# Kernel optimization log

Hardware: AMD Instinct MI355X
Metric: run time of the kernel (lower is better)

The kernel has to match this reference:

```python
import jax, jax.numpy as jnp
import numpy as np

B = 256          # batch_size (number of graphs)
N = 512          # padded nodes per graph
IN_FEATS = 74
DIM = 128
E = 1_048_576    # total edges in batched graph
N_NODES = B * N


def setup_inputs() -> dict:
    key = jax.random.key(0)
    ks = jax.random.split(key, 10)
    x = jax.random.normal(ks[0], (N_NODES, IN_FEATS), dtype=jnp.float32)
    src = jax.random.randint(ks[1], (E,), 0, N_NODES, dtype=jnp.int32)
    dst = jax.random.randint(ks[2], (E,), 0, N_NODES, dtype=jnp.int32)
    # init_transform: Linear(in_feats, dim_embedding, bias=False); padding=True
    # zeroes weight[-1] (last OUTPUT row) -> last column in [in, out] layout.
    W_init = jax.random.normal(ks[3], (IN_FEATS, DIM), dtype=jnp.float32) * 0.1
    W_init = W_init.at[:, -1].set(0.0)
    W1 = jax.random.normal(ks[4], (DIM, DIM), dtype=jnp.float32) * 0.1
    W2 = jax.random.normal(ks[5], (DIM, DIM), dtype=jnp.float32) * 0.1
    W3 = jax.random.normal(ks[6], (DIM, DIM), dtype=jnp.float32) * 0.1
    b1 = jnp.zeros((DIM,), dtype=jnp.float32)
    b2 = jnp.zeros((DIM,), dtype=jnp.float32)
    b3 = jnp.zeros((DIM,), dtype=jnp.float32)
    return {"x": x, "src": src, "dst": dst, "W_init": W_init,
            "W1": W1, "b1": b1, "W2": W2, "b2": b2, "W3": W3, "b3": b3}


def _gcn_forward(x, src, dst, W_init, Ws, bs):
    n = x.shape[0]
    h = x @ W_init                                    # [n, DIM] initial embedding
    ones = jnp.ones(src.shape[0], dtype=x.dtype)
    deg_out = jax.ops.segment_sum(ones, src, num_segments=n)
    deg_in = jax.ops.segment_sum(ones, dst, num_segments=n)
    nrm_src = jax.lax.rsqrt(jnp.clip(deg_out, 1.0))   # D_out^{-1/2}
    nrm_dst = jax.lax.rsqrt(jnp.clip(deg_in, 1.0))    # D_in^{-1/2}
    for W, b in zip(Ws, bs):
        m = (h * nrm_src[:, None])[src]               # gather normalized messages [E, DIM]
        agg = jax.ops.segment_sum(m, dst, num_segments=n)  # scatter-add to dst nodes
        h = jax.nn.relu((agg * nrm_dst[:, None]) @ W + b)
    return h.reshape(B, N, -1)                        # [B, N, output_feats]


def reference(x, src, dst, W_init, W1, b1, W2, b2, W3, b3):
    return _gcn_forward(x, src, dst, W_init, (W1, W2, W3), (b1, b2, b3))
```

## Files before the change

### kernel.cpp

```cpp
#include <hip/hip_runtime.h>

#define NN 131072
#define NE 1048576
#define OFF_DEG_OUT 0x000000
#define OFF_CURSOR  0x080000
#define OFF_WT      0x100000
#define OFF_WTI     0x118000
#define OFF_BUCKET  0x200000
#define OFF_HN      0x2200000
#define OFF_SCA     0x3200000
#define OFF_SCB     0x3280000

typedef __attribute__((ext_vector_type(8))) short bf16x8;
typedef __attribute__((ext_vector_type(4))) float f32x4;

static __device__ __forceinline__ float blo(unsigned u){ return __uint_as_float(u << 16); }
static __device__ __forceinline__ float bhi(unsigned u){ return __uint_as_float(u & 0xffff0000u); }
static __device__ __forceinline__ unsigned f2b(float f){
    unsigned u = __float_as_uint(f);
    return (u + 0x7fffu + ((u >> 16) & 1u)) >> 16;
}
static __device__ __forceinline__ unsigned pack2(float a, float b){
    return f2b(a) | (f2b(b) << 16);
}
static __device__ __forceinline__ unsigned packq(int q0, int q1, int q2, int q3){
    return (q0 & 255) | ((q1 & 255) << 8) | ((q2 & 255) << 16) | ((q3 & 255) << 24);
}

__global__ __launch_bounds__(256) void k_wprep(const float* __restrict__ W1,
                                               const float* __restrict__ W2,
                                               const float* __restrict__ W3,
                                               const float* __restrict__ Wi,
                                               unsigned short* __restrict__ Wt,
                                               unsigned short* __restrict__ Wti,
                                               uint4* __restrict__ zdst) {
    int idx = blockIdx.x * 256 + threadIdx.x;
    zdst[idx] = (uint4){0u, 0u, 0u, 0u};
    if (idx < 49152) {
        int L = idx >> 14, rem = idx & 16383;
        int k = rem >> 7, n = rem & 127;
        const float* W = L == 0 ? W1 : (L == 1 ? W2 : W3);
        Wt[L * 16384 + n * 128 + k] = (unsigned short)f2b(W[k * 128 + n]);
    } else if (idx < 61440) {
        int rem = idx - 49152;
        int n = rem / 96, k = rem - n * 96;
        float v = (k < 74) ? Wi[k * 128 + n] : 0.f;
        Wti[n * 96 + k] = (unsigned short)f2b(v);
    }
}

__global__ __launch_bounds__(256) void k_pre(const int* __restrict__ src,
                                             const int* __restrict__ dst,
                                             int* __restrict__ deg_out,
                                             int* __restrict__ cursor,
                                             int* __restrict__ bucket,
                                             const float* __restrict__ X,
                                             const unsigned short* __restrict__ Wti,
                                             unsigned char* __restrict__ hn,
                                             float* __restrict__ scInv) {
    __shared__ unsigned int xs[64 * 68];
    int tid = threadIdx.x;

    if (!(blockIdx.x & 1)) {
        int base = ((blockIdx.x >> 1) * 256 + tid) * 2;
        int2 s2 = *(const int2*)&src[base];
        int2 d2 = *(const int2*)&dst[base];
        int p0 = atomicAdd(&cursor[d2.x], 1);
        int p1 = atomicAdd(&cursor[d2.y], 1);
        atomicAdd(&deg_out[s2.x], 1);
        atomicAdd(&deg_out[s2.y], 1);
        if (p0 < 64) bucket[(size_t)d2.x * 64 + p0] = s2.x;
        if (p1 < 64) bucket[(size_t)d2.y * 64 + p1] = s2.y;
        return;
    }

    int m0 = (blockIdx.x >> 1) * 64;

    for (int idx = tid; idx < 2368; idx += 256) {
        int m = idx / 37, t = idx - m * 37;
        float2 v = *(const float2*)&X[(size_t)(m0 + m) * 74 + t * 2];
        xs[m * 68 + t] = pack2(v.x, v.y);
    }
    for (int idx = tid; idx < 64 * 11; idx += 256) {
        int m = idx / 11, c = 37 + idx % 11;
        xs[m * 68 + c] = 0u;
    }
    __syncthreads();

    int wave = tid >> 6, lane = tid & 63, quad = lane >> 4, l16 = lane & 15;
    f32x4 acc[8];
    #pragma unroll
    for (int t = 0; t < 8; ++t) acc[t] = (f32x4){0.f, 0.f, 0.f, 0.f};
    int arow = (wave * 16 + l16) * 68 + quad * 4;
    #pragma unroll
    for (int ks = 0; ks < 3; ++ks) {
        bf16x8 af = *(const bf16x8*)&xs[arow + ks * 16];
        #pragma unroll
        for (int t = 0; t < 8; ++t) {
            bf16x8 bf = *(const bf16x8*)(Wti + (t * 16 + l16) * 96 + ks * 32 + quad * 8);
            acc[t] = __builtin_amdgcn_mfma_f32_16x16x32_bf16(af, bf, acc[t], 0, 0, 0);
        }
    }
    __syncthreads();
    unsigned short* atb = (unsigned short*)xs;
    int mb = wave * 16 + quad * 4;
    #pragma unroll
    for (int t = 0; t < 8; ++t)
        #pragma unroll
        for (int r = 0; r < 4; ++r)
            atb[(mb + r) * 136 + t * 16 + l16] = (unsigned short)f2b(acc[t][r]);
    __syncthreads();
    {
        int r = tid >> 2, cg = tid & 3;
        const unsigned int* sp = &xs[r * 68 + cg * 16];
        float v[32]; float am = 0.f;
        #pragma unroll
        for (int j = 0; j < 16; ++j) {
            unsigned u = sp[j];
            float e = blo(u), o = bhi(u);
            v[2 * j] = e; v[2 * j + 1] = o;
            am = fmaxf(am, fmaxf(fabsf(e), fabsf(o)));
        }
        am = fmaxf(am, __shfl_xor(am, 1));
        am = fmaxf(am, __shfl_xor(am, 2));
        float scl = am > 1e-30f ? 127.f / am : 0.f;
        if (cg == 0) scInv[m0 + r] = am * (1.f / 127.f);
        unsigned w[8];
        #pragma unroll
        for (int j = 0; j < 8; ++j)
            w[j] = packq((int)rintf(v[4 * j] * scl),     (int)rintf(v[4 * j + 1] * scl),
                         (int)rintf(v[4 * j + 2] * scl), (int)rintf(v[4 * j + 3] * scl));
        uint4* op = (uint4*)(hn + (size_t)(m0 + r) * 128 + cg * 32);
        op[0] = (uint4){w[0], w[1], w[2], w[3]};
        op[1] = (uint4){w[4], w[5], w[6], w[7]};
    }
}

__global__ __launch_bounds__(256) void k_scnorm(float* __restrict__ sc,
                                                const int* __restrict__ deg) {
    int i = blockIdx.x * 256 + threadIdx.x;
    int d = deg[i];
    sc[i] *= rsqrtf((float)(d > 1 ? d : 1));
}

#define DEQS8(vv, ss) do {                                                     \
    unsigned ux = (vv).x, uy = (vv).y;                                         \
    a0 = fmaf((ss), (float)(int)(signed char)(ux),       a0);                  \
    a1 = fmaf((ss), (float)(int)(signed char)(ux >> 8),  a1);                  \
    a2 = fmaf((ss), (float)(int)(signed char)(ux >> 16), a2);                  \
    a3 = fmaf((ss), (float)(int)(signed char)(ux >> 24), a3);                  \
    a4 = fmaf((ss), (float)(int)(signed char)(uy),       a4);                  \
    a5 = fmaf((ss), (float)(int)(signed char)(uy >> 8),  a5);                  \
    a6 = fmaf((ss), (float)(int)(signed char)(uy >> 16), a6);                  \
    a7 = fmaf((ss), (float)(int)(signed char)(uy >> 24), a7);                  \
} while (0)

#define DEQU8(vv, ss) do {                                                     \
    unsigned ux = (vv).x, uy = (vv).y;                                         \
    a0 = fmaf((ss), (float)(ux & 255),         a0);                            \
    a1 = fmaf((ss), (float)((ux >> 8) & 255),  a1);                            \
    a2 = fmaf((ss), (float)((ux >> 16) & 255), a2);                            \
    a3 = fmaf((ss), (float)(ux >> 24),         a3);                            \
    a4 = fmaf((ss), (float)(uy & 255),         a4);                            \
    a5 = fmaf((ss), (float)((uy >> 8) & 255),  a5);                            \
    a6 = fmaf((ss), (float)((uy >> 16) & 255), a6);                            \
    a7 = fmaf((ss), (float)(uy >> 24),         a7);                            \
} while (0)

template<int USRC>
__global__ __launch_bounds__(256) void k_layer(const uint2* __restrict__ hn2,
                                               const float* __restrict__ sc,
                                               const int* __restrict__ bucket,
                                               const int* __restrict__ deg_in,
                                               const int* __restrict__ deg_out,
                                               const unsigned short* __restrict__ Wt,
                                               const float* __restrict__ bias,
                                               void* __restrict__ OutP,
                                               float* __restrict__ scOut, int last) {
    __shared__ unsigned int at[64 * 68];
    int tid = threadIdx.x;
    int m0 = blockIdx.x * 64;

    int g = tid >> 4, l16p = tid & 15;
    #pragma unroll
    for (int pass = 0; pass < 4; ++pass) {
        int nl = pass * 16 + g;
        int n = m0 + nl;
        int cnt = deg_in[n];
        cnt = cnt < 64 ? cnt : 64;
        const int* brow = bucket + (size_t)n * 64;
        float a0 = 0, a1 = 0, a2 = 0, a3 = 0, a4 = 0, a5 = 0, a6 = 0, a7 = 0;
        for (int c = 0; c < cnt; c += 8) {
            int4 sA = *(const int4*)&brow[c];
            int4 sB = *(const int4*)&brow[c + 4];
            int lim = cnt - c;
            int i1 = lim > 1 ? sA.y : 0;
            int i2 = lim > 2 ? sA.z : 0;
            int i3 = lim > 3 ? sA.w : 0;
            int i4 = lim > 4 ? sB.x : 0;
            int i5 = lim > 5 ? sB.y : 0;
            int i6 = lim > 6 ? sB.z : 0;
            int i7 = lim > 7 ? sB.w : 0;
            uint2 v0 = hn2[(size_t)sA.x * 16 + l16p];
            uint2 v1 = hn2[(size_t)i1 * 16 + l16p];
            uint2 v2 = hn2[(size_t)i2 * 16 + l16p];
            uint2 v3 = hn2[(size_t)i3 * 16 + l16p];
            uint2 v4 = hn2[(size_t)i4 * 16 + l16p];
            uint2 v5 = hn2[(size_t)i5 * 16 + l16p];
            uint2 v6 = hn2[(size_t)i6 * 16 + l16p];
            uint2 v7 = hn2[(size_t)i7 * 16 + l16p];
            float s0 = sc[sA.x];
            float s1 = sc[i1]; s1 = lim > 1 ? s1 : 0.f;
            float s2 = sc[i2]; s2 = lim > 2 ? s2 : 0.f;
            float s3 = sc[i3]; s3 = lim > 3 ? s3 : 0.f;
            float s4 = sc[i4]; s4 = lim > 4 ? s4 : 0.f;
            float s5 = sc[i5]; s5 = lim > 5 ? s5 : 0.f;
            float s6 = sc[i6]; s6 = lim > 6 ? s6 : 0.f;
            float s7 = sc[i7]; s7 = lim > 7 ? s7 : 0.f;
            if (USRC) {
                DEQU8(v0, s0); DEQU8(v1, s1); DEQU8(v2, s2); DEQU8(v3, s3);
                DEQU8(v4, s4); DEQU8(v5, s5); DEQU8(v6, s6); DEQU8(v7, s7);
            } else {
                DEQS8(v0, s0); DEQS8(v1, s1); DEQS8(v2, s2); DEQS8(v3, s3);
                DEQS8(v4, s4); DEQS8(v5, s5); DEQS8(v6, s6); DEQS8(v7, s7);
            }
        }
        float nd = rsqrtf((float)(cnt > 1 ? cnt : 1));
        uint4 o;
        o.x = pack2(a0 * nd, a1 * nd); o.y = pack2(a2 * nd, a3 * nd);
        o.z = pack2(a4 * nd, a5 * nd); o.w = pack2(a6 * nd, a7 * nd);
        *(uint4*)&at[nl * 68 + l16p * 4] = o;
    }
    __syncthreads();

    f32x4 acc[8];
    #pragma unroll
    for (int t = 0; t < 8; ++t) acc[t] = (f32x4){0.f, 0.f, 0.f, 0.f};
    int wave = tid >> 6, lane = tid & 63, quad = lane >> 4, l16 = lane & 15;
    int arow = (wave * 16 + l16) * 68 + quad * 4;
    #pragma unroll
    for (int ks = 0; ks < 4; ++ks) {
        bf16x8 af = *(const bf16x8*)&at[arow + ks * 16];
        #pragma unroll
        for (int t = 0; t < 8; ++t) {
            bf16x8 bf = *(const bf16x8*)(Wt + (t * 16 + l16) * 128 + ks * 32 + quad * 8);
            acc[t] = __builtin_amdgcn_mfma_f32_16x16x32_bf16(af, bf, acc[t], 0, 0, 0);
        }
    }

    int mb = wave * 16 + quad * 4;
    if (!last) {
        float nsr[4];
        #pragma unroll
        for (int r = 0; r < 4; ++r) {
            int dq = deg_out[m0 + mb + r];
            nsr[r] = rsqrtf((float)(dq > 1 ? dq : 1));
        }
        __syncthreads();
        unsigned short* atb = (unsigned short*)at;
        #pragma unroll
        for (int t = 0; t < 8; ++t) {
            float bv = bias[t * 16 + l16];
            #pragma unroll
            for (int r = 0; r < 4; ++r) {
                float v = acc[t][r] + bv;
                v = (v > 0.f ? v : 0.f) * nsr[r];
                atb[(mb + r) * 136 + t * 16 + l16] = (unsigned short)f2b(v);
            }
        }
        __syncthreads();
        int r = tid >> 2, cg = tid & 3;
        const unsigned int* sp = &at[r * 68 + cg * 16];
        float v[32]; float am = 0.f;
        #pragma unroll
        for (int j = 0; j < 16; ++j) {
            unsigned u = sp[j];
            float e = blo(u), o = bhi(u);
            v[2 * j] = e; v[2 * j + 1] = o;
            am = fmaxf(am, fmaxf(e, o));
        }
        am = fmaxf(am, __shfl_xor(am, 1));
        am = fmaxf(am, __shfl_xor(am, 2));
        float scl = am > 1e-30f ? 254.f / am : 0.f;
        if (cg == 0) scOut[m0 + r] = am * (1.f / 254.f);
        unsigned w[8];
        #pragma unroll
        for (int j = 0; j < 8; ++j)
            w[j] = packq((int)rintf(v[4 * j] * scl),     (int)rintf(v[4 * j + 1] * scl),
                         (int)rintf(v[4 * j + 2] * scl), (int)rintf(v[4 * j + 3] * scl));
        unsigned char* Out = (unsigned char*)OutP;
        uint4* op = (uint4*)(Out + (size_t)(m0 + r) * 128 + cg * 32);
        op[0] = (uint4){w[0], w[1], w[2], w[3]};
        op[1] = (uint4){w[4], w[5], w[6], w[7]};
    } else {
        float* Out = (float*)OutP;
        #pragma unroll
        for (int t = 0; t < 8; ++t) {
            float bv = bias[t * 16 + l16];
            #pragma unroll
            for (int r = 0; r < 4; ++r) {
                float v = acc[t][r] + bv;
                v = v > 0.f ? v : 0.f;
                Out[(size_t)(m0 + mb + r) * 128 + t * 16 + l16] = v;
            }
        }
    }
}

extern "C" void kernel_launch(void* const* d_in, const int* in_sizes, int n_in,
                              void* d_out, int out_size, void* d_ws, size_t ws_size,
                              hipStream_t stream) {
    const float* x  = (const float*)d_in[0];
    const int* src  = (const int*)d_in[1];
    const int* dst  = (const int*)d_in[2];
    const float* Wi = (const float*)d_in[3];
    const float* W1 = (const float*)d_in[4];
    const float* b1 = (const float*)d_in[5];
    const float* W2 = (const float*)d_in[6];
    const float* b2 = (const float*)d_in[7];
    const float* W3 = (const float*)d_in[8];
    const float* b3 = (const float*)d_in[9];

    char* ws = (char*)d_ws;
    int* deg_out   = (int*)(ws + OFF_DEG_OUT);
    int* cursor    = (int*)(ws + OFF_CURSOR);
    unsigned short* Wt  = (unsigned short*)(ws + OFF_WT);
    unsigned short* Wti = (unsigned short*)(ws + OFF_WTI);
    int* bucket    = (int*)(ws + OFF_BUCKET);
    unsigned char* hnA = (unsigned char*)(ws + OFF_HN);
    float* scA     = (float*)(ws + OFF_SCA);
    float* scB     = (float*)(ws + OFF_SCB);
    unsigned char* hnB = (unsigned char*)d_out;

    k_wprep<<<256, 256, 0, stream>>>(W1, W2, W3, Wi, Wt, Wti, (uint4*)ws);
    k_pre<<<4096, 256, 0, stream>>>(src, dst, deg_out, cursor, bucket, x, Wti, hnA, scA);
    k_scnorm<<<NN / 256, 256, 0, stream>>>(scA, deg_out);

    k_layer<0><<<NN / 64, 256, 0, stream>>>((const uint2*)hnA, scA, bucket, cursor, deg_out,
                                            Wt,         b1, (void*)hnB, scB, 0);
    k_layer<1><<<NN / 64, 256, 0, stream>>>((const uint2*)hnB, scB, bucket, cursor, deg_out,
                                            Wt + 16384, b2, (void*)hnA, scA, 0);
    k_layer<1><<<NN / 64, 256, 0, stream>>>((const uint2*)hnA, scA, bucket, cursor, deg_out,
                                            Wt + 32768, b3, d_out, nullptr, 1);
}
```

Baseline: 392.1 us.

## Requantize features to a global scale to drop per-source scale gathers

```diff
diff --git a/kernel.cpp b/kernel.cpp
--- a/kernel.cpp
+++ b/kernel.cpp
@@ -8,8 +8,9 @@
 #define OFF_WTI     0x118000
 #define OFF_BUCKET  0x200000
 #define OFF_HN      0x2200000
-#define OFF_SCA     0x3200000
-#define OFF_SCB     0x3280000
+#define OFF_SCA     0x3210000
+#define OFF_SCB     0x3290000
+#define OFF_GMAX    0x3310000
 
 typedef __attribute__((ext_vector_type(8))) short bf16x8;
 typedef __attribute__((ext_vector_type(4))) float f32x4;
@@ -33,9 +34,19 @@
                                                const float* __restrict__ Wi,
                                                unsigned short* __restrict__ Wt,
                                                unsigned short* __restrict__ Wti,
-                                               uint4* __restrict__ zdst) {
+                                               uint4* __restrict__ zdst,
+                                               unsigned char* __restrict__ hnA,
+                                               unsigned char* __restrict__ hnB,
+                                               unsigned int* __restrict__ gmax) {
     int idx = blockIdx.x * 256 + threadIdx.x;
     zdst[idx] = (uint4){0u, 0u, 0u, 0u};
+    if (blockIdx.x == 255) {
+        int t = threadIdx.x;
+        uint4 z = (uint4){0u, 0u, 0u, 0u};
+        if (t < 8)        ((uint4*)(hnA + (size_t)NN * 128))[t] = z;
+        else if (t < 16)  ((uint4*)(hnB + (size_t)NN * 128))[t - 8] = z;
+        else if (t == 16) { gmax[0] = 0u; gmax[1] = 0u; gmax[2] = 0u; }
+    }
     if (idx < 49152) {
         int L = idx >> 14, rem = idx & 16383;
         int k = rem >> 7, n = rem & 127;
@@ -136,50 +147,98 @@
     }
 }
 
-__global__ __launch_bounds__(256) void k_scnorm(float* __restrict__ sc,
-                                                const int* __restrict__ deg) {
+__global__ __launch_bounds__(256) void k_mkgs0(const float* __restrict__ sc,
+                                               const int* __restrict__ deg,
+                                               unsigned int* __restrict__ gmax) {
     int i = blockIdx.x * 256 + threadIdx.x;
     int d = deg[i];
-    sc[i] *= rsqrtf((float)(d > 1 ? d : 1));
-}
-
-#define DEQS8(vv, ss) do {                                                     \
+    float s = sc[i] * 127.f * rsqrtf((float)(d > 1 ? d : 1));
+    s = fmaxf(s, __shfl_xor(s, 1));
+    s = fmaxf(s, __shfl_xor(s, 2));
+    s = fmaxf(s, __shfl_xor(s, 4));
+    s = fmaxf(s, __shfl_xor(s, 8));
+    s = fmaxf(s, __shfl_xor(s, 16));
+    s = fmaxf(s, __shfl_xor(s, 32));
+    if ((threadIdx.x & 63) == 0) atomicMax(gmax, __float_as_uint(s));
+}
+
+template<int SIGNED>
+__global__ __launch_bounds__(256) void k_requant(unsigned int* __restrict__ hnW,
+                                                 const float* __restrict__ sc,
+                                                 const int* __restrict__ deg,
+                                                 const unsigned int* __restrict__ gmax) {
+    int gid = blockIdx.x * 256 + threadIdx.x;
+    int r = gid >> 3;
+    float g = fmaxf(__uint_as_float(gmax[0]), 1e-30f);
+    float f;
+    if (SIGNED) {
+        int d = deg[r];
+        f = sc[r] * rsqrtf((float)(d > 1 ? d : 1)) * (127.f / g);
+    } else {
+        f = sc[r] * (254.f / g);
+    }
+    uint4 v = ((const uint4*)hnW)[gid];
+    unsigned w[4]; unsigned vv[4] = {v.x, v.y, v.z, v.w};
+    #pragma unroll
+    for (int j = 0; j < 4; ++j) {
+        unsigned u = vv[j];
+        int q0, q1, q2, q3;
+        if (SIGNED) {
+            q0 = (int)rintf((float)(int)(signed char)(u)       * f);
+            q1 = (int)rintf((float)(int)(signed char)(u >> 8)  * f);
+            q2 = (int)rintf((float)(int)(signed char)(u >> 16) * f);
+            q3 = (int)rintf((float)(int)(signed char)(u >> 24) * f);
+        } else {
+            q0 = (int)rintf((float)(u & 255)         * f);
+            q1 = (int)rintf((float)((u >> 8) & 255)  * f);
+            q2 = (int)rintf((float)((u >> 16) & 255) * f);
+            q3 = (int)rintf((float)(u >> 24)         * f);
+        }
+        w[j] = packq(q0, q1, q2, q3);
+    }
+    ((uint4*)hnW)[gid] = (uint4){w[0], w[1], w[2], w[3]};
+}
+
+#define ACCS8(vv) do {                                                         \
     unsigned ux = (vv).x, uy = (vv).y;                                         \
-    a0 = fmaf((ss), (float)(int)(signed char)(ux),       a0);                  \
-    a1 = fmaf((ss), (float)(int)(signed char)(ux >> 8),  a1);                  \
-    a2 = fmaf((ss), (float)(int)(signed char)(ux >> 16), a2);                  \
-    a3 = fmaf((ss), (float)(int)(signed char)(ux >> 24), a3);                  \
-    a4 = fmaf((ss), (float)(int)(signed char)(uy),       a4);                  \
-    a5 = fmaf((ss), (float)(int)(signed char)(uy >> 8),  a5);                  \
-    a6 = fmaf((ss), (float)(int)(signed char)(uy >> 16), a6);                  \
-    a7 = fmaf((ss), (float)(int)(signed char)(uy >> 24), a7);                  \
+    a0 += (float)(int)(signed char)(ux);                                       \
+    a1 += (float)(int)(signed char)(ux >> 8);                                  \
+    a2 += (float)(int)(signed char)(ux >> 16);                                 \
+    a3 += (float)(int)(signed char)(ux >> 24);                                 \
+    a4 += (float)(int)(signed char)(uy);                                       \
+    a5 += (float)(int)(signed char)(uy >> 8);                                  \
+    a6 += (float)(int)(signed char)(uy >> 16);                                 \
+    a7 += (float)(int)(signed char)(uy >> 24);                                 \
 } while (0)
 
-#define DEQU8(vv, ss) do {                                                     \
+#define ACCU8(vv) do {                                                         \
     unsigned ux = (vv).x, uy = (vv).y;                                         \
-    a0 = fmaf((ss), (float)(ux & 255),         a0);                            \
-    a1 = fmaf((ss), (float)((ux >> 8) & 255),  a1);                            \
-    a2 = fmaf((ss), (float)((ux >> 16) & 255), a2);                            \
-    a3 = fmaf((ss), (float)(ux >> 24),         a3);                            \
-    a4 = fmaf((ss), (float)(uy & 255),         a4);                            \
-    a5 = fmaf((ss), (float)((uy >> 8) & 255),  a5);                            \
-    a6 = fmaf((ss), (float)((uy >> 16) & 255), a6);                            \
-    a7 = fmaf((ss), (float)(uy >> 24),         a7);                            \
+    a0 += (float)(ux & 255);                                                   \
+    a1 += (float)((ux >> 8) & 255);                                            \
+    a2 += (float)((ux >> 16) & 255);                                           \
+    a3 += (float)(ux >> 24);                                                   \
+    a4 += (float)(uy & 255);                                                   \
+    a5 += (float)((uy >> 8) & 255);                                            \
+    a6 += (float)((uy >> 16) & 255);                                           \
+    a7 += (float)(uy >> 24);                                                   \
 } while (0)
 
 template<int USRC>
 __global__ __launch_bounds__(256) void k_layer(const uint2* __restrict__ hn2,
-                                               const float* __restrict__ sc,
+                                               const unsigned int* __restrict__ gmaxIn,
                                                const int* __restrict__ bucket,
                                                const int* __restrict__ deg_in,
                                                const int* __restrict__ deg_out,
                                                const unsigned short* __restrict__ Wt,
                                                const float* __restrict__ bias,
                                                void* __restrict__ OutP,
-                                               float* __restrict__ scOut, int last) {
+                                               float* __restrict__ scOut,
+                                               unsigned int* __restrict__ gmaxOut,
+                                               int last) {
     __shared__ unsigned int at[64 * 68];
     int tid = threadIdx.x;
     int m0 = blockIdx.x * 64;
+    float gs = __uint_as_float(gmaxIn[0]) * (USRC ? 1.f / 254.f : 1.f / 127.f);
 
     int g = tid >> 4, l16p = tid & 15;
     #pragma unroll
@@ -194,13 +253,13 @@
             int4 sA = *(const int4*)&brow[c];
             int4 sB = *(const int4*)&brow[c + 4];
             int lim = cnt - c;
-            int i1 = lim > 1 ? sA.y : 0;
-            int i2 = lim > 2 ? sA.z : 0;
-            int i3 = lim > 3 ? sA.w : 0;
-            int i4 = lim > 4 ? sB.x : 0;
-            int i5 = lim > 5 ? sB.y : 0;
-            int i6 = lim > 6 ? sB.z : 0;
-            int i7 = lim > 7 ? sB.w : 0;
+            int i1 = lim > 1 ? sA.y : NN;
+            int i2 = lim > 2 ? sA.z : NN;
+            int i3 = lim > 3 ? sA.w : NN;
+            int i4 = lim > 4 ? sB.x : NN;
+            int i5 = lim > 5 ? sB.y : NN;
+            int i6 = lim > 6 ? sB.z : NN;
+            int i7 = lim > 7 ? sB.w : NN;
             uint2 v0 = hn2[(size_t)sA.x * 16 + l16p];
             uint2 v1 = hn2[(size_t)i1 * 16 + l16p];
             uint2 v2 = hn2[(size_t)i2 * 16 + l16p];
@@ -209,23 +268,15 @@
             uint2 v5 = hn2[(size_t)i5 * 16 + l16p];
             uint2 v6 = hn2[(size_t)i6 * 16 + l16p];
             uint2 v7 = hn2[(size_t)i7 * 16 + l16p];
-            float s0 = sc[sA.x];
-            float s1 = sc[i1]; s1 = lim > 1 ? s1 : 0.f;
-            float s2 = sc[i2]; s2 = lim > 2 ? s2 : 0.f;
-            float s3 = sc[i3]; s3 = lim > 3 ? s3 : 0.f;
-            float s4 = sc[i4]; s4 = lim > 4 ? s4 : 0.f;
-            float s5 = sc[i5]; s5 = lim > 5 ? s5 : 0.f;
-            float s6 = sc[i6]; s6 = lim > 6 ? s6 : 0.f;
-            float s7 = sc[i7]; s7 = lim > 7 ? s7 : 0.f;
             if (USRC) {
-                DEQU8(v0, s0); DEQU8(v1, s1); DEQU8(v2, s2); DEQU8(v3, s3);
-                DEQU8(v4, s4); DEQU8(v5, s5); DEQU8(v6, s6); DEQU8(v7, s7);
+                ACCU8(v0); ACCU8(v1); ACCU8(v2); ACCU8(v3);
+                ACCU8(v4); ACCU8(v5); ACCU8(v6); ACCU8(v7);
             } else {
-                DEQS8(v0, s0); DEQS8(v1, s1); DEQS8(v2, s2); DEQS8(v3, s3);
-                DEQS8(v4, s4); DEQS8(v5, s5); DEQS8(v6, s6); DEQS8(v7, s7);
+                ACCS8(v0); ACCS8(v1); ACCS8(v2); ACCS8(v3);
+                ACCS8(v4); ACCS8(v5); ACCS8(v6); ACCS8(v7);
             }
         }
-        float nd = rsqrtf((float)(cnt > 1 ? cnt : 1));
+        float nd = gs * rsqrtf((float)(cnt > 1 ? cnt : 1));
         uint4 o;
         o.x = pack2(a0 * nd, a1 * nd); o.y = pack2(a2 * nd, a3 * nd);
         o.z = pack2(a4 * nd, a5 * nd); o.w = pack2(a6 * nd, a7 * nd);
@@ -283,6 +334,11 @@
         am = fmaxf(am, __shfl_xor(am, 2));
         float scl = am > 1e-30f ? 254.f / am : 0.f;
         if (cg == 0) scOut[m0 + r] = am * (1.f / 254.f);
+        float wm = fmaxf(am, __shfl_xor(am, 4));
+        wm = fmaxf(wm, __shfl_xor(wm, 8));
+        wm = fmaxf(wm, __shfl_xor(wm, 16));
+        wm = fmaxf(wm, __shfl_xor(wm, 32));
+        if ((tid & 63) == 0) atomicMax(gmaxOut, __float_as_uint(wm));
         unsigned w[8];
         #pragma unroll
         for (int j = 0; j < 8; ++j)
@@ -330,16 +386,20 @@
     unsigned char* hnA = (unsigned char*)(ws + OFF_HN);
     float* scA     = (float*)(ws + OFF_SCA);
     float* scB     = (float*)(ws + OFF_SCB);
+    unsigned int* gmax = (unsigned int*)(ws + OFF_GMAX);
     unsigned char* hnB = (unsigned char*)d_out;
 
-    k_wprep<<<256, 256, 0, stream>>>(W1, W2, W3, Wi, Wt, Wti, (uint4*)ws);
+    k_wprep<<<256, 256, 0, stream>>>(W1, W2, W3, Wi, Wt, Wti, (uint4*)ws, hnA, hnB, gmax);
     k_pre<<<4096, 256, 0, stream>>>(src, dst, deg_out, cursor, bucket, x, Wti, hnA, scA);
-    k_scnorm<<<NN / 256, 256, 0, stream>>>(scA, deg_out);
-
-    k_layer<0><<<NN / 64, 256, 0, stream>>>((const uint2*)hnA, scA, bucket, cursor, deg_out,
-                                            Wt,         b1, (void*)hnB, scB, 0);
-    k_layer<1><<<NN / 64, 256, 0, stream>>>((const uint2*)hnB, scB, bucket, cursor, deg_out,
-                                            Wt + 16384, b2, (void*)hnA, scA, 0);
-    k_layer<1><<<NN / 64, 256, 0, stream>>>((const uint2*)hnA, scA, bucket, cursor, deg_out,
-                                            Wt + 32768, b3, d_out, nullptr, 1);
-}
+    k_mkgs0<<<NN / 256, 256, 0, stream>>>(scA, deg_out, gmax);
+    k_requant<1><<<4096, 256, 0, stream>>>((unsigned int*)hnA, scA, deg_out, gmax);
+
+    k_layer<0><<<NN / 64, 256, 0, stream>>>((const uint2*)hnA, gmax, bucket, cursor, deg_out,
+                                            Wt,         b1, (void*)hnB, scB, gmax + 1, 0);
+    k_requant<0><<<4096, 256, 0, stream>>>((unsigned int*)hnB, scB, nullptr, gmax + 1);
+    k_layer<1><<<NN / 64, 256, 0, stream>>>((const uint2*)hnB, gmax + 1, bucket, cursor, deg_out,
+                                            Wt + 16384, b2, (void*)hnA, scA, gmax + 2, 0);
+    k_requant<0><<<4096, 256, 0, stream>>>((unsigned int*)hnA, scA, nullptr, gmax + 2);
+    k_layer<1><<<NN / 64, 256, 0, stream>>>((const uint2*)hnA, gmax + 2, bucket, cursor, deg_out,
+                                            Wt + 32768, b3, d_out, nullptr, nullptr, 1);
+}
```

Result: slower. 520.5 us (+32.8%).
